# Kernel optimization log

Measured on AMD Instinct MI355X. Metric: run time of the kernel, lower is better.

The kernel has to match this reference:

```python
import jax, jax.numpy as jnp
import numpy as np

V = 32000; D = 1024; H = 16; L = 2; T = 2048; B = 4; C = 32000
DH = D // H
EPS = 1e-5


def layernorm(x, g, b):
    mu = jnp.mean(x, axis=-1, keepdims=True)
    var = jnp.mean((x - mu) ** 2, axis=-1, keepdims=True)
    return (x - mu) * jax.lax.rsqrt(var + EPS) * g + b


def setup_inputs() -> dict:
    key = jax.random.key(0)
    ks = jax.random.split(key, 16)
    s = 0.02
    return {
        "tokens": jax.random.randint(ks[0], (B, T), 0, V),
        "embed_W": jax.random.normal(ks[1], (V, D), jnp.float32) * s,
        "pos_W": jax.random.normal(ks[2], (T, D), jnp.float32) * s,
        "ln_g": jnp.ones((L, D), jnp.float32),
        "ln_b": jnp.zeros((L, D), jnp.float32),
        "qkv_W": jax.random.normal(ks[3], (L, D, 3 * D), jnp.float32) * s,
        "qkv_b": jnp.zeros((L, 3 * D), jnp.float32),
        "out_W": jax.random.normal(ks[4], (L, D, D), jnp.float32) * s,
        "out_b": jnp.zeros((L, D), jnp.float32),
        "lnf_g": jnp.ones((D,), jnp.float32),
        "lnf_b": jnp.zeros((D,), jnp.float32),
        "head_W": jax.random.normal(ks[5], (D, C), jnp.float32) * s,
        "head_b": jnp.zeros((C,), jnp.float32),
    }


def attn_block(x, g, b, Wqkv, bqkv, Wo, bo):
    # pre-LN attention + residual. NOTE: original module defines an MLP but never calls it.
    h = layernorm(x, g, b)
    qkv = h @ Wqkv + bqkv                      # [B,T,3D]
    q, k, v = jnp.split(qkv, 3, axis=-1)
    q = q.reshape(B, T, H, DH)
    k = k.reshape(B, T, H, DH)
    v = v.reshape(B, T, H, DH)
    scores = jnp.einsum("bqhd,bkhd->bhqk", q, k) / np.sqrt(DH)
    causal = jnp.tril(jnp.ones((T, T), bool))
    scores = jnp.where(causal, scores, -jnp.inf)
    attn = jax.nn.softmax(scores, axis=-1)
    o = jnp.einsum("bhqk,bkhd->bqhd", attn, v).reshape(B, T, D)
    return x + o @ Wo + bo


def reference(tokens, embed_W, pos_W, ln_g, ln_b, qkv_W, qkv_b, out_W, out_b,
              lnf_g, lnf_b, head_W, head_b):
    h = embed_W[tokens] + pos_W[jnp.arange(T)][None, :, :]   # [B,T,D]
    for i in range(L):
        h = attn_block(h, ln_g[i], ln_b[i], qkv_W[i], qkv_b[i], out_W[i], out_b[i])
    h = layernorm(h, lnf_g, lnf_b)
    logits = h[:, -1] @ head_W + head_b                      # [B,C]
    return logits
```

## Files before the change

kernel.cpp:

```cpp
#include <hip/hip_runtime.h>

typedef __attribute__((ext_vector_type(8))) __bf16 bf16x8;
typedef __attribute__((ext_vector_type(4))) __bf16 bf16x4;
typedef __attribute__((ext_vector_type(4))) float f32x4;
typedef unsigned long long ull;

static constexpr int kB = 4, kT = 2048, kD = 1024, kH = 16;
static constexpr int kC = 32000, kM = 8192, k3D = 3072, kQK = 2048;

#define MFMA16(a, b, c) __builtin_amdgcn_mfma_f32_16x16x32_bf16((a), (b), (c), 0, 0, 0)

__device__ __forceinline__ void gload_lds16(const __bf16* g, __bf16* l) {
  __builtin_amdgcn_global_load_lds(
      (const __attribute__((address_space(1))) unsigned int*)(const void*)g,
      (__attribute__((address_space(3))) unsigned int*)(void*)l, 16, 0, 0);
}

__global__ __launch_bounds__(256) void embed_ln_kernel(const int* __restrict__ tok,
                                                       const float* __restrict__ embW,
                                                       const float* __restrict__ posW,
                                                       const float* __restrict__ g,
                                                       const float* __restrict__ bb,
                                                       float* __restrict__ h,
                                                       __bf16* __restrict__ hn) {
  const int row = blockIdx.x, tid = threadIdx.x;
  const int t = row & (kT - 1);
  const int tk = tok[row];
  const f32x4 e = ((const f32x4*)(embW + (size_t)tk * kD))[tid];
  const f32x4 p = ((const f32x4*)(posW + (size_t)t * kD))[tid];
  const f32x4 xv = e + p;
  ((f32x4*)(h + (size_t)row * kD))[tid] = xv;
  float s  = xv[0] + xv[1] + xv[2] + xv[3];
  float s2 = xv[0]*xv[0] + xv[1]*xv[1] + xv[2]*xv[2] + xv[3]*xv[3];
  #pragma unroll
  for (int off = 1; off < 64; off <<= 1) {
    s  += __shfl_xor(s, off);
    s2 += __shfl_xor(s2, off);
  }
  __shared__ float red[8];
  const int w = tid >> 6;
  if ((tid & 63) == 0) { red[w*2] = s; red[w*2+1] = s2; }
  __syncthreads();
  s  = red[0] + red[2] + red[4] + red[6];
  s2 = red[1] + red[3] + red[5] + red[7];
  const float mu  = s * (1.f / kD);
  const float var = s2 * (1.f / kD) - mu * mu;
  const float rs  = rsqrtf(var + 1e-5f);
  const f32x4 gv = ((const f32x4*)g)[tid];
  const f32x4 bv = ((const f32x4*)bb)[tid];
  bf16x4 o;
  #pragma unroll
  for (int i = 0; i < 4; i++) o[i] = (__bf16)((xv[i] - mu) * rs * gv[i] + bv[i]);
  ((bf16x4*)(hn + (size_t)row * kD))[tid] = o;
}

template <bool BF16OUT>
__global__ __launch_bounds__(256) void ln_kernel(const float* __restrict__ x,
                                                 const float* __restrict__ g,
                                                 const float* __restrict__ bb,
                                                 void* __restrict__ outp) {
  const int row = blockIdx.x, tid = threadIdx.x;
  const f32x4 xv = ((const f32x4*)(x + (size_t)row * kD))[tid];
  float s  = xv[0] + xv[1] + xv[2] + xv[3];
  float s2 = xv[0]*xv[0] + xv[1]*xv[1] + xv[2]*xv[2] + xv[3]*xv[3];
  #pragma unroll
  for (int off = 1; off < 64; off <<= 1) {
    s  += __shfl_xor(s, off);
    s2 += __shfl_xor(s2, off);
  }
  __shared__ float red[8];
  const int w = tid >> 6;
  if ((tid & 63) == 0) { red[w*2] = s; red[w*2+1] = s2; }
  __syncthreads();
  s  = red[0] + red[2] + red[4] + red[6];
  s2 = red[1] + red[3] + red[5] + red[7];
  const float mu  = s * (1.f / kD);
  const float var = s2 * (1.f / kD) - mu * mu;
  const float rs  = rsqrtf(var + 1e-5f);
  const f32x4 gv = ((const f32x4*)g)[tid];
  const f32x4 bv = ((const f32x4*)bb)[tid];
  if constexpr (BF16OUT) {
    bf16x4 o;
    #pragma unroll
    for (int i = 0; i < 4; i++) o[i] = (__bf16)((xv[i] - mu) * rs * gv[i] + bv[i]);
    ((bf16x4*)((__bf16*)outp + (size_t)row * kD))[tid] = o;
  } else {
    f32x4 o;
    #pragma unroll
    for (int i = 0; i < 4; i++) o[i] = (xv[i] - mu) * rs * gv[i] + bv[i];
    ((f32x4*)((float*)outp + (size_t)row * kD))[tid] = o;
  }
}

__global__ __launch_bounds__(256) void transpose_all_kernel(const float* __restrict__ qkv_W,
                                                            const float* __restrict__ out_W,
                                                            __bf16* __restrict__ WqkvT,
                                                            __bf16* __restrict__ WoT) {
  __shared__ float sh[32][33];
  const int bid = blockIdx.x;
  const float* W; __bf16* WT; int N, tile;
  if (bid < 3072)      { W = qkv_W;                   WT = WqkvT;                    N = k3D; tile = bid; }
  else if (bid < 6144) { W = qkv_W + (size_t)kD*k3D;  WT = WqkvT + (size_t)k3D*kD;   N = k3D; tile = bid - 3072; }
  else                 { W = out_W;                   WT = WoT;                      N = kD;  tile = bid - 6144; }
  const int tx = threadIdx.x & 31, ty = threadIdx.x >> 5;
  const int ntile = N >> 5;
  const int c0 = (tile % ntile) << 5;
  const int r0 = (tile / ntile) << 5;
  #pragma unroll
  for (int i = 0; i < 4; i++) {
    const int r = ty + i * 8;
    sh[r][tx] = W[(size_t)(r0 + r) * N + c0 + tx];
  }
  __syncthreads();
  #pragma unroll
  for (int i = 0; i < 4; i++) {
    const int cc = ty + i * 8;
    WT[(size_t)(c0 + cc) * kD + r0 + tx] = (__bf16)sh[tx][cc];
  }
}

template <bool OUT_BF16>
__global__ __launch_bounds__(256) void gemm_bt_kernel(const __bf16* __restrict__ A,
                                                      const __bf16* __restrict__ BT,
                                                      const float* __restrict__ bias,
                                                      const float* resid,
                                                      float* outf,
                                                      __bf16* outb,
                                                      __bf16* vtp,
                                                      int N, int K, int ldc, int vt_c0,
                                                      int bm_mult, int bm_add) {
  __shared__ __bf16 As[128 * 64];
  __shared__ __bf16 Bs[128 * 64];
  const int tid = threadIdx.x;
  const int lane = tid & 63, w = tid >> 6;
  int wg = (int)blockIdx.x;
  const int nwg = gridDim.x;
  wg = (wg & 7) * (nwg >> 3) + (wg >> 3);
  const int nbn = N >> 7;
  const int bm = (wg / nbn) * bm_mult + bm_add;
  const int bn = wg % nbn;
  const int wr = (w >> 1) * 64, wc = (w & 1) * 64;
  const int lrow = lane & 15, lk8 = (lane >> 4) * 8;

  const int srow = lane >> 3;
  const int scol = (lane & 7) * 8;
  const __bf16* gA = A + (size_t)(bm * 128) * K;
  const __bf16* gB = BT + (size_t)(bn * 128) * K;

  f32x4 acc[4][4] = {};

  for (int k0 = 0; k0 < K; k0 += 64) {
    __syncthreads();
    #pragma unroll
    for (int i = 0; i < 4; i++) {
      const int c = w * 4 + i;
      const int row = c * 8 + srow;
      gload_lds16(gA + (size_t)row * K + k0 + scol, As + c * 512);
      gload_lds16(gB + (size_t)row * K + k0 + scol, Bs + c * 512);
    }
    __syncthreads();
    #pragma unroll
    for (int ks = 0; ks < 2; ks++) {
      bf16x8 af[4], bf[4];
      #pragma unroll
      for (int mt = 0; mt < 4; mt++)
        af[mt] = *(const bf16x8*)(As + (wr + mt * 16 + lrow) * 64 + ks * 32 + lk8);
      #pragma unroll
      for (int nt = 0; nt < 4; nt++)
        bf[nt] = *(const bf16x8*)(Bs + (wc + nt * 16 + lrow) * 64 + ks * 32 + lk8);
      __builtin_amdgcn_s_setprio(1);
      #pragma unroll
      for (int mt = 0; mt < 4; mt++)
        #pragma unroll
        for (int nt = 0; nt < 4; nt++)
          acc[mt][nt] = MFMA16(af[mt], bf[nt], acc[mt][nt]);
      __builtin_amdgcn_s_setprio(0);
    }
  }

  #pragma unroll
  for (int mt = 0; mt < 4; mt++) {
    const int row0 = bm * 128 + wr + mt * 16 + (lane >> 4) * 4;
    #pragma unroll
    for (int nt = 0; nt < 4; nt++) {
      const int col = bn * 128 + wc + nt * 16 + lrow;
      const float bsv = bias[col];
      if (vtp && col >= vt_c0) {
        const int vd = col - vt_c0;
        const int bb_ = row0 >> 11, t = row0 & (kT - 1);
        bf16x4 pk;
        #pragma unroll
        for (int r = 0; r < 4; r++) pk[r] = (__bf16)(acc[mt][nt][r] + bsv);
        *(bf16x4*)(vtp + ((size_t)((bb_ << 4) + (vd >> 6)) * 64 + (vd & 63)) * kT + t) = pk;
      } else {
        #pragma unroll
        for (int r = 0; r < 4; r++) {
          const size_t idx = (size_t)(row0 + r) * ldc + col;
          const float v = acc[mt][nt][r] + bsv;
          if constexpr (OUT_BF16) {
            outb[idx] = (__bf16)v;
          } else {
            outf[idx] = v + resid[idx];
          }
        }
      }
    }
  }
}

template <int MODE>
__global__ __launch_bounds__(256) void flash_kernel(const __bf16* __restrict__ qkv,
                                                    const __bf16* __restrict__ vtg,
                                                    __bf16* __restrict__ o,
                                                    float* __restrict__ part_acc,
                                                    float* __restrict__ part_ml,
                                                    int nsub) {
  constexpr float SC = 0.18033688011112042f;
  __shared__ __bf16 Qs[64 * 64];
  __shared__ __bf16 Ks[2][64 * 64];
  __shared__ __bf16 Vs[2][64 * 64];
  const int tid = threadIdx.x, lane = tid & 63, w = tid >> 6;
  int wg = (int)blockIdx.x;
  const int nwg = gridDim.x;
  wg = (wg & 7) * (nwg >> 3) + (wg >> 3);
  const int sub = wg % nsub, bh = wg / nsub;
  const int b = bh >> 4, hh = bh & 15;
  const int g = lane >> 4, qown = lane & 15;
  const int sslot = (lane & 7) ^ ((lane >> 3) & 7);
  const int swz = (qown & 7) << 3;
  const size_t row0 = (size_t)b * kT;
  const int NS = (MODE == 0) ? 2 : 1;
  const int r8 = lane >> 3;

  for (int s = 0; s < NS; s++) {
    int qt, ktlo, kthi;
    if constexpr (MODE == 0) {
      qt = s ? (2 * nsub - 1 - sub) : sub;
      ktlo = 0; kthi = qt + 1;
    } else {
      qt = 31; ktlo = sub * 4; kthi = ktlo + 4;
    }

    __syncthreads();
    #pragma unroll
    for (int j = 0; j < 2; j++) {
      const int r = w * 16 + j * 8 + r8;
      gload_lds16(qkv + (row0 + qt * 64 + r) * kQK + hh * 64 + sslot * 8,
                  Qs + (w * 16 + j * 8) * 64);
      gload_lds16(qkv + (row0 + ktlo * 64 + r) * kQK + 1024 + hh * 64 + sslot * 8,
                  Ks[0] + (w * 16 + j * 8) * 64);
      gload_lds16(vtg + ((size_t)bh * 64 + r) * kT + ktlo * 64 + sslot * 8,
                  Vs[0] + (w * 16 + j * 8) * 64);
    }
    __syncthreads();
    bf16x8 qf[2];
    #pragma unroll
    for (int ks = 0; ks < 2; ks++) {
      bf16x8 qr = *(const bf16x8*)(Qs + (w * 16 + qown) * 64 + ((ks * 32 + 8 * g) ^ swz));
      #pragma unroll
      for (int i = 0; i < 8; i++) qf[ks][i] = (__bf16)((float)qr[i] * SC);
    }

    float m_run = -1e30f, l_run = 0.f;
    f32x4 acc[4] = {};
    int cur = 0;

    for (int kt = ktlo; kt < kthi; kt++) {
      if (kt + 1 < kthi) {
        #pragma unroll
        for (int j = 0; j < 2; j++) {
          const int r = w * 16 + j * 8 + r8;
          gload_lds16(qkv + (row0 + (kt + 1) * 64 + r) * kQK + 1024 + hh * 64 + sslot * 8,
                      Ks[cur ^ 1] + (w * 16 + j * 8) * 64);
          gload_lds16(vtg + ((size_t)bh * 64 + r) * kT + (kt + 1) * 64 + sslot * 8,
                      Vs[cur ^ 1] + (w * 16 + j * 8) * 64);
        }
      }

      f32x4 sv[4] = {};
      __builtin_amdgcn_s_setprio(1);
      #pragma unroll
      for (int nt = 0; nt < 4; nt++) {
        const int kr = nt * 16 + qown;
        #pragma unroll
        for (int ks = 0; ks < 2; ks++) {
          bf16x8 kf = *(const bf16x8*)(Ks[cur] + kr * 64 + ((ks * 32 + 8 * g) ^ swz));
          sv[nt] = MFMA16(kf, qf[ks], sv[nt]);
        }
      }
      __builtin_amdgcn_s_setprio(0);
      if (kt == qt) {
        #pragma unroll
        for (int nt = 0; nt < 4; nt++)
          #pragma unroll
          for (int r = 0; r < 4; r++)
            if (nt * 16 + 4 * g + r > w * 16 + qown) sv[nt][r] = -1e30f;
      }

      float mx = -1e30f;
      #pragma unroll
      for (int nt = 0; nt < 4; nt++)
        #pragma unroll
        for (int r = 0; r < 4; r++) mx = fmaxf(mx, sv[nt][r]);
      mx = fmaxf(mx, __shfl_xor(mx, 16));
      mx = fmaxf(mx, __shfl_xor(mx, 32));

      float ps = 0.f;
      ull quad[4];
      if (__all(mx - m_run <= 8.0f)) {
        #pragma unroll
        for (int nt = 0; nt < 4; nt++) {
          union { bf16x4 v; ull u; } qd;
          #pragma unroll
          for (int r = 0; r < 4; r++) {
            const float p = exp2f(sv[nt][r] - m_run);
            ps += p;
            qd.v[r] = (__bf16)p;
          }
          quad[nt] = qd.u;
        }
        ps += __shfl_xor(ps, 16);
        ps += __shfl_xor(ps, 32);
        l_run += ps;
      } else {
        const float mnew = fmaxf(m_run, mx);
        const float fsc = exp2f(m_run - mnew);
        m_run = mnew;
        #pragma unroll
        for (int nt = 0; nt < 4; nt++) {
          union { bf16x4 v; ull u; } qd;
          #pragma unroll
          for (int r = 0; r < 4; r++) {
            const float p = exp2f(sv[nt][r] - mnew);
            ps += p;
            qd.v[r] = (__bf16)p;
          }
          quad[nt] = qd.u;
        }
        ps += __shfl_xor(ps, 16);
        ps += __shfl_xor(ps, 32);
        l_run = l_run * fsc + ps;
        float fr[4];
        #pragma unroll
        for (int r = 0; r < 4; r++) fr[r] = __shfl(fsc, 20 * g + r);
        #pragma unroll
        for (int nt = 0; nt < 4; nt++)
          #pragma unroll
          for (int r = 0; r < 4; r++) acc[nt][r] *= fr[r];
      }

      bf16x8 pf[2];
      #pragma unroll
      for (int ks = 0; ks < 2; ks++) {
        const int src = (g & 1) * 32 + qown;
        const ull t0 = __shfl(quad[2 * ks],     src);
        const ull t1 = __shfl(quad[2 * ks + 1], src);
        const ull lo = (g & 2) ? t1 : t0;
        const ull t2 = __shfl(quad[2 * ks],     src + 16);
        const ull t3 = __shfl(quad[2 * ks + 1], src + 16);
        const ull hi = (g & 2) ? t3 : t2;
        union { ull u[2]; bf16x8 v; } pk;
        pk.u[0] = lo; pk.u[1] = hi;
        pf[ks] = pk.v;
      }

      __builtin_amdgcn_s_setprio(1);
      #pragma unroll
      for (int nt = 0; nt < 4; nt++) {
        const int vr = nt * 16 + qown;
        #pragma unroll
        for (int ks = 0; ks < 2; ks++) {
          bf16x8 vf = *(const bf16x8*)(Vs[cur] + vr * 64 + ((ks * 32 + 8 * g) ^ swz));
          acc[nt] = MFMA16(pf[ks], vf, acc[nt]);
        }
      }
      __builtin_amdgcn_s_setprio(0);

      __syncthreads();
      cur ^= 1;
    }

    if constexpr (MODE == 0) {
      const float li = 1.f / l_run;
      float lr[4];
      #pragma unroll
      for (int r = 0; r < 4; r++) lr[r] = __shfl(li, 20 * g + r);
      #pragma unroll
      for (int r = 0; r < 4; r++) {
        const int t = qt * 64 + w * 16 + 4 * g + r;
        #pragma unroll
        for (int nt = 0; nt < 4; nt++)
          o[(row0 + t) * kD + hh * 64 + nt * 16 + qown] = (__bf16)(acc[nt][r] * lr[r]);
      }
    } else {
      const int tile = bh * nsub + sub;
      #pragma unroll
      for (int r = 0; r < 4; r++) {
        const int rr = w * 16 + 4 * g + r;
        #pragma unroll
        for (int nt = 0; nt < 4; nt++)
          part_acc[(size_t)tile * 4096 + rr * 64 + nt * 16 + qown] = acc[nt][r];
      }
      if (g == 0) {
        part_ml[tile * 128 + w * 16 + qown] = m_run;
        part_ml[tile * 128 + 64 + w * 16 + qown] = l_run;
      }
    }
  }
}

__global__ __launch_bounds__(256) void flash_merge_kernel(const float* __restrict__ part_acc,
                                                          const float* __restrict__ part_ml,
                                                          __bf16* __restrict__ o) {
  const int bh = blockIdx.x, b = bh >> 4, hh = bh & 15;
  for (int e = threadIdx.x; e < 4096; e += 256) {
    const int row = e >> 6, d = e & 63;
    float mstar = -1e30f;
    #pragma unroll
    for (int kc = 0; kc < 8; kc++)
      mstar = fmaxf(mstar, part_ml[(bh * 8 + kc) * 128 + row]);
    float lstar = 0.f, osum = 0.f;
    #pragma unroll
    for (int kc = 0; kc < 8; kc++) {
      const float wgt = exp2f(part_ml[(bh * 8 + kc) * 128 + row] - mstar);
      lstar += wgt * part_ml[(bh * 8 + kc) * 128 + 64 + row];
      osum  += wgt * part_acc[(size_t)(bh * 8 + kc) * 4096 + e];
    }
    o[(size_t)(b * kT + 1984 + row) * kD + hh * 64 + d] = (__bf16)(osum / lstar);
  }
}

__global__ __launch_bounds__(256) void proj_last_kernel(const __bf16* __restrict__ o,
                                                        const float* __restrict__ W,
                                                        const float* __restrict__ bias,
                                                        const float* __restrict__ h,
                                                        float* __restrict__ out4) {
  const int b = blockIdx.y;
  const int j = blockIdx.x * 256 + threadIdx.x;
  __shared__ float ov[kD];
  const __bf16* orow = o + (size_t)(b * kT + kT - 1) * kD;
  for (int i = threadIdx.x; i < kD; i += 256) ov[i] = (float)orow[i];
  __syncthreads();
  float acc = 0.f;
  #pragma unroll 8
  for (int k = 0; k < kD; k++) acc = fmaf(ov[k], W[(size_t)k * kD + j], acc);
  out4[b * kD + j] = h[(size_t)(b * kT + kT - 1) * kD + j] + bias[j] + acc;
}

__global__ __launch_bounds__(256) void head_kernel(const float* __restrict__ hl,
                                                   const float* __restrict__ W,
                                                   const float* __restrict__ hb,
                                                   float* __restrict__ out) {
  const int jj = threadIdx.x & 63, ks = threadIdx.x >> 6;
  const int j = blockIdx.x * 64 + jj;
  __shared__ float sh[kB * kD];
  __shared__ float red[4][kB][64];
  for (int i = threadIdx.x; i < kB * kD; i += 256) sh[i] = hl[i];
  __syncthreads();
  float a[kB] = {};
  const int k0 = ks * 256;
  #pragma unroll 4
  for (int k = k0; k < k0 + 256; k++) {
    const float wv = W[(size_t)k * kC + j];
    #pragma unroll
    for (int bb = 0; bb < kB; bb++) a[bb] = fmaf(sh[bb * kD + k], wv, a[bb]);
  }
  #pragma unroll
  for (int bb = 0; bb < kB; bb++) red[ks][bb][jj] = a[bb];
  __syncthreads();
  if (ks == 0) {
    const float bv = hb[j];
    #pragma unroll
    for (int bb = 0; bb < kB; bb++)
      out[(size_t)bb * kC + j] = red[0][bb][jj] + red[1][bb][jj] + red[2][bb][jj] + red[3][bb][jj] + bv;
  }
}

extern "C" void kernel_launch(void* const* d_in, const int* in_sizes, int n_in,
                              void* d_out, int out_size, void* d_ws, size_t ws_size,
                              hipStream_t stream) {
  const int*   tokens = (const int*)d_in[0];
  const float* embW   = (const float*)d_in[1];
  const float* posW   = (const float*)d_in[2];
  const float* ln_g   = (const float*)d_in[3];
  const float* ln_b   = (const float*)d_in[4];
  const float* qkv_W  = (const float*)d_in[5];
  const float* qkv_b  = (const float*)d_in[6];
  const float* out_W  = (const float*)d_in[7];
  const float* out_b  = (const float*)d_in[8];
  const float* lnf_g  = (const float*)d_in[9];
  const float* lnf_b  = (const float*)d_in[10];
  const float* headW  = (const float*)d_in[11];
  const float* headb  = (const float*)d_in[12];
  float* logits = (float*)d_out;

  char* ws = (char*)d_ws;
  float*  h     = (float*)(ws);
  __bf16* hn    = (__bf16*)(ws + 33554432);
  __bf16* qkv   = (__bf16*)(ws + 50331648);
  __bf16* Vt    = (__bf16*)(ws + 83886080);
  __bf16* ob    = (__bf16*)(ws + 100663296);
  __bf16* WqkvT = (__bf16*)(ws + 117440512);
  __bf16* WoT   = (__bf16*)(ws + 130613248);
  float*  hl4   = (float*)(ws + 132710400);
  float*  hl    = (float*)(ws + 132726784);
  float* part_acc = (float*)(ws + 33554432);
  float* part_ml  = (float*)(ws + 33554432 + 8388608);

  transpose_all_kernel<<<7168, 256, 0, stream>>>(qkv_W, out_W, WqkvT, WoT);
  embed_ln_kernel<<<kM, 256, 0, stream>>>(tokens, embW, posW, ln_g, ln_b, h, hn);

  gemm_bt_kernel<true><<<(kM/128)*(k3D/128), 256, 0, stream>>>(
      hn, WqkvT, qkv_b, nullptr, nullptr, qkv, Vt, k3D, kD, kQK, 2048, 1, 0);
  flash_kernel<0><<<kB*kH*16, 256, 0, stream>>>(qkv, Vt, ob, nullptr, nullptr, 16);
  gemm_bt_kernel<false><<<(kM/128)*(kD/128), 256, 0, stream>>>(
      ob, WoT, out_b, h, h, nullptr, nullptr, kD, kD, kD, 1 << 30, 1, 0);

  ln_kernel<true><<<kM, 256, 0, stream>>>(h, ln_g + kD, ln_b + kD, hn);
  gemm_bt_kernel<true><<<(kM/128)*(2048/128), 256, 0, stream>>>(
      hn, WqkvT + (size_t)k3D*kD + (size_t)kD*kD, qkv_b + k3D + kD,
      nullptr, nullptr, qkv + 1024, Vt, 2048, kD, kQK, 1024, 1, 0);
  gemm_bt_kernel<true><<<kB*(kD/128), 256, 0, stream>>>(
      hn, WqkvT + (size_t)k3D*kD, qkv_b + k3D,
      nullptr, nullptr, qkv, nullptr, kD, kD, kQK, 1 << 30, 16, 15);
  flash_kernel<1><<<kB*kH*8, 256, 0, stream>>>(qkv, Vt, nullptr, part_acc, part_ml, 8);
  flash_merge_kernel<<<kB*kH, 256, 0, stream>>>(part_acc, part_ml, ob);
  proj_last_kernel<<<dim3(kD/256, kB), 256, 0, stream>>>(ob, out_W + (size_t)kD*kD,
                                                         out_b + kD, h, hl4);

  ln_kernel<false><<<kB, 256, 0, stream>>>(hl4, lnf_g, lnf_b, hl);
  head_kernel<<<500, 256, 0, stream>>>(hl, headW, headb, logits);
}
```

Measured before the change: 480.8 us.

## Single-buffer flash attention with one query tile per workgroup

Result: no change. 486.6 us (+1.2%).

```diff
diff --git a/kernel.cpp b/kernel.cpp
--- a/kernel.cpp
+++ b/kernel.cpp
@@ -217,8 +217,8 @@
                                                     int nsub) {
   constexpr float SC = 0.18033688011112042f;
   __shared__ __bf16 Qs[64 * 64];
-  __shared__ __bf16 Ks[2][64 * 64];
-  __shared__ __bf16 Vs[2][64 * 64];
+  __shared__ __bf16 Ks[64 * 64];
+  __shared__ __bf16 Vs[64 * 64];
   const int tid = threadIdx.x, lane = tid & 63, w = tid >> 6;
   int wg = (int)blockIdx.x;
   const int nwg = gridDim.x;
@@ -229,182 +229,166 @@
   const int sslot = (lane & 7) ^ ((lane >> 3) & 7);
   const int swz = (qown & 7) << 3;
   const size_t row0 = (size_t)b * kT;
-  const int NS = (MODE == 0) ? 2 : 1;
   const int r8 = lane >> 3;
 
-  for (int s = 0; s < NS; s++) {
-    int qt, ktlo, kthi;
-    if constexpr (MODE == 0) {
-      qt = s ? (2 * nsub - 1 - sub) : sub;
-      ktlo = 0; kthi = qt + 1;
-    } else {
-      qt = 31; ktlo = sub * 4; kthi = ktlo + 4;
-    }
-
+  int qt, ktlo, kthi;
+  if constexpr (MODE == 0) {
+    qt = nsub - 1 - sub;
+    ktlo = 0; kthi = qt + 1;
+  } else {
+    qt = 31; ktlo = sub * 4; kthi = ktlo + 4;
+  }
+
+  #pragma unroll
+  for (int j = 0; j < 2; j++) {
+    const int r = w * 16 + j * 8 + r8;
+    gload_lds16(qkv + (row0 + qt * 64 + r) * kQK + hh * 64 + sslot * 8,
+                Qs + (w * 16 + j * 8) * 64);
+  }
+  __syncthreads();
+  bf16x8 qf[2];
+  #pragma unroll
+  for (int ks = 0; ks < 2; ks++) {
+    bf16x8 qr = *(const bf16x8*)(Qs + (w * 16 + qown) * 64 + ((ks * 32 + 8 * g) ^ swz));
+    #pragma unroll
+    for (int i = 0; i < 8; i++) qf[ks][i] = (__bf16)((float)qr[i] * SC);
+  }
+
+  float m_run = -1e30f, l_run = 0.f;
+  f32x4 acc[4] = {};
+
+  for (int kt = ktlo; kt < kthi; kt++) {
     __syncthreads();
     #pragma unroll
     for (int j = 0; j < 2; j++) {
       const int r = w * 16 + j * 8 + r8;
-      gload_lds16(qkv + (row0 + qt * 64 + r) * kQK + hh * 64 + sslot * 8,
-                  Qs + (w * 16 + j * 8) * 64);
-      gload_lds16(qkv + (row0 + ktlo * 64 + r) * kQK + 1024 + hh * 64 + sslot * 8,
-                  Ks[0] + (w * 16 + j * 8) * 64);
-      gload_lds16(vtg + ((size_t)bh * 64 + r) * kT + ktlo * 64 + sslot * 8,
-                  Vs[0] + (w * 16 + j * 8) * 64);
+      gload_lds16(qkv + (row0 + kt * 64 + r) * kQK + 1024 + hh * 64 + sslot * 8,
+                  Ks + (w * 16 + j * 8) * 64);
+      gload_lds16(vtg + ((size_t)bh * 64 + r) * kT + kt * 64 + sslot * 8,
+                  Vs + (w * 16 + j * 8) * 64);
     }
     __syncthreads();
-    bf16x8 qf[2];
+
+    f32x4 sv[4] = {};
+    #pragma unroll
+    for (int nt = 0; nt < 4; nt++) {
+      const int kr = nt * 16 + qown;
+      #pragma unroll
+      for (int ks = 0; ks < 2; ks++) {
+        bf16x8 kf = *(const bf16x8*)(Ks + kr * 64 + ((ks * 32 + 8 * g) ^ swz));
+        sv[nt] = MFMA16(kf, qf[ks], sv[nt]);
+      }
+    }
+    if (kt == qt) {
+      #pragma unroll
+      for (int nt = 0; nt < 4; nt++)
+        #pragma unroll
+        for (int r = 0; r < 4; r++)
+          if (nt * 16 + 4 * g + r > w * 16 + qown) sv[nt][r] = -1e30f;
+    }
+
+    float mx = -1e30f;
+    #pragma unroll
+    for (int nt = 0; nt < 4; nt++)
+      #pragma unroll
+      for (int r = 0; r < 4; r++) mx = fmaxf(mx, sv[nt][r]);
+    mx = fmaxf(mx, __shfl_xor(mx, 16));
+    mx = fmaxf(mx, __shfl_xor(mx, 32));
+
+    float ps = 0.f;
+    ull quad[4];
+    if (__all(mx - m_run <= 8.0f)) {
+      #pragma unroll
+      for (int nt = 0; nt < 4; nt++) {
+        union { bf16x4 v; ull u; } qd;
+        #pragma unroll
+        for (int r = 0; r < 4; r++) {
+          const float p = exp2f(sv[nt][r] - m_run);
+          ps += p;
+          qd.v[r] = (__bf16)p;
+        }
+        quad[nt] = qd.u;
+      }
+      ps += __shfl_xor(ps, 16);
+      ps += __shfl_xor(ps, 32);
+      l_run += ps;
+    } else {
+      const float mnew = fmaxf(m_run, mx);
+      const float fsc = exp2f(m_run - mnew);
+      m_run = mnew;
+      #pragma unroll
+      for (int nt = 0; nt < 4; nt++) {
+        union { bf16x4 v; ull u; } qd;
+        #pragma unroll
+        for (int r = 0; r < 4; r++) {
+          const float p = exp2f(sv[nt][r] - mnew);
+          ps += p;
+          qd.v[r] = (__bf16)p;
+        }
+        quad[nt] = qd.u;
+      }
+      ps += __shfl_xor(ps, 16);
+      ps += __shfl_xor(ps, 32);
+      l_run = l_run * fsc + ps;
+      float fr[4];
+      #pragma unroll
+      for (int r = 0; r < 4; r++) fr[r] = __shfl(fsc, 20 * g + r);
+      #pragma unroll
+      for (int nt = 0; nt < 4; nt++)
+        #pragma unroll
+        for (int r = 0; r < 4; r++) acc[nt][r] *= fr[r];
+    }
+
+    bf16x8 pf[2];
     #pragma unroll
     for (int ks = 0; ks < 2; ks++) {
-      bf16x8 qr = *(const bf16x8*)(Qs + (w * 16 + qown) * 64 + ((ks * 32 + 8 * g) ^ swz));
-      #pragma unroll
-      for (int i = 0; i < 8; i++) qf[ks][i] = (__bf16)((float)qr[i] * SC);
-    }
-
-    float m_run = -1e30f, l_run = 0.f;
-    f32x4 acc[4] = {};
-    int cur = 0;
-
-    for (int kt = ktlo; kt < kthi; kt++) {
-      if (kt + 1 < kthi) {
-        #pragma unroll
-        for (int j = 0; j < 2; j++) {
-          const int r = w * 16 + j * 8 + r8;
-          gload_lds16(qkv + (row0 + (kt + 1) * 64 + r) * kQK + 1024 + hh * 64 + sslot * 8,
-                      Ks[cur ^ 1] + (w * 16 + j * 8) * 64);
-          gload_lds16(vtg + ((size_t)bh * 64 + r) * kT + (kt + 1) * 64 + sslot * 8,
-                      Vs[cur ^ 1] + (w * 16 + j * 8) * 64);
-        }
+      const int src = (g & 1) * 32 + qown;
+      const ull t0 = __shfl(quad[2 * ks],     src);
+      const ull t1 = __shfl(quad[2 * ks + 1], src);
+      const ull lo = (g & 2) ? t1 : t0;
+      const ull t2 = __shfl(quad[2 * ks],     src + 16);
+      const ull t3 = __shfl(quad[2 * ks + 1], src + 16);
+      const ull hi = (g & 2) ? t3 : t2;
+      union { ull u[2]; bf16x8 v; } pk;
+      pk.u[0] = lo; pk.u[1] = hi;
+      pf[ks] = pk.v;
+    }
+
+    #pragma unroll
+    for (int nt = 0; nt < 4; nt++) {
+      const int vr = nt * 16 + qown;
+      #pragma unroll
+      for (int ks = 0; ks < 2; ks++) {
+        bf16x8 vf = *(const bf16x8*)(Vs + vr * 64 + ((ks * 32 + 8 * g) ^ swz));
+        acc[nt] = MFMA16(pf[ks], vf, acc[nt]);
       }
-
-      f32x4 sv[4] = {};
-      __builtin_amdgcn_s_setprio(1);
-      #pragma unroll
-      for (int nt = 0; nt < 4; nt++) {
-        const int kr = nt * 16 + qown;
-        #pragma unroll
-        for (int ks = 0; ks < 2; ks++) {
-          bf16x8 kf = *(const bf16x8*)(Ks[cur] + kr * 64 + ((ks * 32 + 8 * g) ^ swz));
-          sv[nt] = MFMA16(kf, qf[ks], sv[nt]);
-        }
-      }
-      __builtin_amdgcn_s_setprio(0);
-      if (kt == qt) {
-        #pragma unroll
-        for (int nt = 0; nt < 4; nt++)
-          #pragma unroll
-          for (int r = 0; r < 4; r++)
-            if (nt * 16 + 4 * g + r > w * 16 + qown) sv[nt][r] = -1e30f;
-      }
-
-      float mx = -1e30f;
+    }
+  }
+
+  if constexpr (MODE == 0) {
+    const float li = 1.f / l_run;
+    float lr[4];
+    #pragma unroll
+    for (int r = 0; r < 4; r++) lr[r] = __shfl(li, 20 * g + r);
+    #pragma unroll
+    for (int r = 0; r < 4; r++) {
+      const int t = qt * 64 + w * 16 + 4 * g + r;
       #pragma unroll
       for (int nt = 0; nt < 4; nt++)
-        #pragma unroll
-        for (int r = 0; r < 4; r++) mx = fmaxf(mx, sv[nt][r]);
-      mx = fmaxf(mx, __shfl_xor(mx, 16));
-      mx = fmaxf(mx, __shfl_xor(mx, 32));
-
-      float ps = 0.f;
-      ull quad[4];
-      if (__all(mx - m_run <= 8.0f)) {
-        #pragma unroll
-        for (int nt = 0; nt < 4; nt++) {
-          union { bf16x4 v; ull u; } qd;
-          #pragma unroll
-          for (int r = 0; r < 4; r++) {
-            const float p = exp2f(sv[nt][r] - m_run);
-            ps += p;
-            qd.v[r] = (__bf16)p;
-          }
-          quad[nt] = qd.u;
-        }
-        ps += __shfl_xor(ps, 16);
-        ps += __shfl_xor(ps, 32);
-        l_run += ps;
-      } else {
-        const float mnew = fmaxf(m_run, mx);
-        const float fsc = exp2f(m_run - mnew);
-        m_run = mnew;
-        #pragma unroll
-        for (int nt = 0; nt < 4; nt++) {
-          union { bf16x4 v; ull u; } qd;
-          #pragma unroll
-          for (int r = 0; r < 4; r++) {
-            const float p = exp2f(sv[nt][r] - mnew);
-            ps += p;
-            qd.v[r] = (__bf16)p;
-          }
-          quad[nt] = qd.u;
-        }
-        ps += __shfl_xor(ps, 16);
-        ps += __shfl_xor(ps, 32);
-        l_run = l_run * fsc + ps;
-        float fr[4];
-        #pragma unroll
-        for (int r = 0; r < 4; r++) fr[r] = __shfl(fsc, 20 * g + r);
-        #pragma unroll
-        for (int nt = 0; nt < 4; nt++)
-          #pragma unroll
-          for (int r = 0; r < 4; r++) acc[nt][r] *= fr[r];
-      }
-
-      bf16x8 pf[2];
-      #pragma unroll
-      for (int ks = 0; ks < 2; ks++) {
-        const int src = (g & 1) * 32 + qown;
-        const ull t0 = __shfl(quad[2 * ks],     src);
-        const ull t1 = __shfl(quad[2 * ks + 1], src);
-        const ull lo = (g & 2) ? t1 : t0;
-        const ull t2 = __shfl(quad[2 * ks],     src + 16);
-        const ull t3 = __shfl(quad[2 * ks + 1], src + 16);
-        const ull hi = (g & 2) ? t3 : t2;
-        union { ull u[2]; bf16x8 v; } pk;
-        pk.u[0] = lo; pk.u[1] = hi;
-        pf[ks] = pk.v;
-      }
-
-      __builtin_amdgcn_s_setprio(1);
-      #pragma unroll
-      for (int nt = 0; nt < 4; nt++) {
-        const int vr = nt * 16 + qown;
-        #pragma unroll
-        for (int ks = 0; ks < 2; ks++) {
-          bf16x8 vf = *(const bf16x8*)(Vs[cur] + vr * 64 + ((ks * 32 + 8 * g) ^ swz));
-          acc[nt] = MFMA16(pf[ks], vf, acc[nt]);
-        }
-      }
-      __builtin_amdgcn_s_setprio(0);
-
-      __syncthreads();
-      cur ^= 1;
-    }
-
-    if constexpr (MODE == 0) {
-      const float li = 1.f / l_run;
-      float lr[4];
-      #pragma unroll
-      for (int r = 0; r < 4; r++) lr[r] = __shfl(li, 20 * g + r);
-      #pragma unroll
-      for (int r = 0; r < 4; r++) {
-        const int t = qt * 64 + w * 16 + 4 * g + r;
-        #pragma unroll
-        for (int nt = 0; nt < 4; nt++)
-          o[(row0 + t) * kD + hh * 64 + nt * 16 + qown] = (__bf16)(acc[nt][r] * lr[r]);
-      }
-    } else {
-      const int tile = bh * nsub + sub;
-      #pragma unroll
-      for (int r = 0; r < 4; r++) {
-        const int rr = w * 16 + 4 * g + r;
-        #pragma unroll
-        for (int nt = 0; nt < 4; nt++)
-          part_acc[(size_t)tile * 4096 + rr * 64 + nt * 16 + qown] = acc[nt][r];
-      }
-      if (g == 0) {
-        part_ml[tile * 128 + w * 16 + qown] = m_run;
-        part_ml[tile * 128 + 64 + w * 16 + qown] = l_run;
-      }
+        o[(row0 + t) * kD + hh * 64 + nt * 16 + qown] = (__bf16)(acc[nt][r] * lr[r]);
+    }
+  } else {
+    const int tile = bh * nsub + sub;
+    #pragma unroll
+    for (int r = 0; r < 4; r++) {
+      const int rr = w * 16 + 4 * g + r;
+      #pragma unroll
+      for (int nt = 0; nt < 4; nt++)
+        part_acc[(size_t)tile * 4096 + rr * 64 + nt * 16 + qown] = acc[nt][r];
+    }
+    if (g == 0) {
+      part_ml[tile * 128 + w * 16 + qown] = m_run;
+      part_ml[tile * 128 + 64 + w * 16 + qown] = l_run;
     }
   }
 }
@@ -512,7 +496,7 @@
 
   gemm_bt_kernel<true><<<(kM/128)*(k3D/128), 256, 0, stream>>>(
       hn, WqkvT, qkv_b, nullptr, nullptr, qkv, Vt, k3D, kD, kQK, 2048, 1, 0);
-  flash_kernel<0><<<kB*kH*16, 256, 0, stream>>>(qkv, Vt, ob, nullptr, nullptr, 16);
+  flash_kernel<0><<<kB*kH*32, 256, 0, stream>>>(qkv, Vt, ob, nullptr, nullptr, 32);
   gemm_bt_kernel<false><<<(kM/128)*(kD/128), 256, 0, stream>>>(
       ob, WoT, out_b, h, h, nullptr, nullptr, kD, kD, kD, 1 << 30, 1, 0);
 
```
